# Optimization experiments

Hardware: AMD Instinct MI355X
Metric: run time of the kernel (lower is better)

Reference implementation:

```python
import jax, jax.numpy as jnp
import numpy as np

T, D, H, E = 8192, 1024, 512, 8
BLK = 32  # MXFP8 scaling block size along the contraction dim


def setup_inputs() -> dict:
    key = jax.random.key(0)
    k1, k2, k3, k4 = jax.random.split(key, 4)
    # qdata: values representable-ish in e4m3 (we use small normal floats)
    output_e4m3 = jax.random.normal(k1, (T, D), dtype=jnp.float32)
    # e8m0 scales are powers of two, one per 32-element block along dim
    output_scales_e8m0 = jnp.exp2(
        jax.random.randint(k2, (T, D // BLK), -2, 3).astype(jnp.float32)
    )
    # uniform token distribution across experts (tokens are expert-contiguous)
    num_tokens_per_expert = jnp.full((E,), T // E, dtype=jnp.int32)
    expert_padded_offsets = jnp.zeros((E,), dtype=jnp.int32)  # unused by forward body
    w13 = jax.random.normal(k3, (E, 2 * H, D), dtype=jnp.float32) * 0.02
    w2 = jax.random.normal(k4, (E, D, H), dtype=jnp.float32) * 0.02
    return {
        "output_e4m3": output_e4m3,
        "output_scales_e8m0": output_scales_e8m0,
        "num_tokens_per_expert": num_tokens_per_expert,
        "expert_padded_offsets": expert_padded_offsets,
        "w13": w13,
        "w2": w2,
    }


def reference(output_e4m3, output_scales_e8m0, num_tokens_per_expert,
              expert_padded_offsets, w13, w2):
    # Dequantize MXFP8: qdata * per-block e8m0 scale, blocks of 32 along dim.
    scales = jnp.repeat(output_scales_e8m0, BLK, axis=-1)  # [T, D]
    x = output_e4m3 * scales  # [T, D] high-precision reference activations
    # Grouped GEMM 1: tokens are expert-contiguous with uniform group sizes,
    # so the ragged grouped matmul reduces to a batched einsum per expert.
    tpe = T // E
    xg = x.reshape(E, tpe, D)                       # [E, tpe, D]
    h13 = jnp.einsum("etd,ehd->eth", xg, w13)       # [E, tpe, 2H]
    h1, h3 = h13[..., :H], h13[..., H:]
    h = jax.nn.silu(h1) * h3                        # fused SiLU-gate
    # Grouped GEMM 2
    out = jnp.einsum("eth,edh->etd", h, w2)         # [E, tpe, D]
    return out.reshape(T, D)
```

## Files before the change

### kernel.cpp

```cpp
#include <hip/hip_runtime.h>
#include <hip/hip_bf16.h>

#define T_TOK 8192
#define DDIM  1024
#define HDIM  512
#define NE    8
#define TPE   (T_TOK / NE)

typedef __attribute__((ext_vector_type(4))) float floatx4;
typedef __attribute__((ext_vector_type(8))) short bf16x8;

#define SBAR() __builtin_amdgcn_sched_barrier(0)

__device__ __forceinline__ unsigned short f2bf(float f) {
    union { float f; unsigned int u; } v;
    v.f = f;
    unsigned int u = v.u;
    unsigned int r = u + 0x7FFFu + ((u >> 16) & 1u);
    return (unsigned short)(r >> 16);
}

__device__ __forceinline__ unsigned int cvt_pk_bf16(float lo, float hi) {
    unsigned int r;
    asm("v_cvt_pk_bf16_f32 %0, %1, %2" : "=v"(r) : "v"(lo), "v"(hi));
    return r;
}

__device__ __forceinline__ void gld_lds16(const void* g, void* l) {
    __builtin_amdgcn_global_load_lds(
        (const __attribute__((address_space(1))) unsigned int*)g,
        (__attribute__((address_space(3))) unsigned int*)l, 16, 0, 0);
}

__global__ __launch_bounds__(256)
void convert_x_kernel(const float* __restrict__ X, const float* __restrict__ S,
                      unsigned short* __restrict__ Xb)
{
    const int NTX = (T_TOK * DDIM) / 4;
    const int stride = gridDim.x * blockDim.x;
    for (int i = blockIdx.x * blockDim.x + threadIdx.x; i < NTX; i += stride) {
        int row = i >> 8;
        int c4  = i & 255;
        float4 v = reinterpret_cast<const float4*>(X)[i];
        float sc = S[row * (DDIM / 32) + (c4 >> 3)];
        ushort4 b;
        b.x = f2bf(v.x * sc); b.y = f2bf(v.y * sc);
        b.z = f2bf(v.z * sc); b.w = f2bf(v.w * sc);
        reinterpret_cast<ushort4*>(Xb)[i] = b;
    }
}

__device__ __forceinline__ int xcd_swizzle_512(int raw) {
    return (raw & 7) * 64 + (raw >> 3);
}


__global__ __launch_bounds__(256, 2)
void gemm1_silu_kernel(const unsigned short* __restrict__ Xb,
                       const float* __restrict__ W13,
                       __hip_bfloat16* __restrict__ Hout)
{
    const int bid = xcd_swizzle_512(blockIdx.x);
    const int e  = bid >> 6;
    const int mt = (bid >> 3) & 7;
    const int nt = bid & 7;
    const int tok0 = e * TPE + mt * 128;
    const float* __restrict__ We = W13 + (size_t)e * (2 * HDIM) * DDIM;

    __shared__ __hip_bfloat16 sA[2][128][64];
    __shared__ __hip_bfloat16 sB[2][128][64];

    const int tid  = threadIdx.x;
    const int lane = tid & 63;
    const int wave = tid >> 6;
    const int wr = wave >> 1;
    const int wc = wave & 1;
    const int lr = lane & 15;
    const int sw0 = ((lane >> 4) ^ (lane & 7));

    floatx4 acc1[4][2] = {};
    floatx4 acc3[4][2] = {};

    const int srow0 = (tid >> 3);
    const int c8    = (tid & 7) * 8;
    const int dcol  = (tid & 7) * 8;
    const int gcol  = ((tid & 7) ^ (srow0 & 7)) * 8;
    const int swcol = gcol;

    float4 rB0[8], rB1[8];

    auto LOADB = [&](int kk, float4* rB) {
        const int k0 = kk * 64;
        #pragma unroll
        for (int j = 0; j < 4; ++j) {
            int row = srow0 + j * 32;
            int wrow = (j < 2) ? (nt * 64 + row)
                               : (HDIM + nt * 64 + (row - 64));
            const float* p = &We[(size_t)wrow * DDIM + k0 + c8];
            rB[2*j]   = *reinterpret_cast<const float4*>(p);
            rB[2*j+1] = *reinterpret_cast<const float4*>(p + 4);
        }
    };
    auto STAGEA = [&](int kk, int buf) {
        const int k0 = kk * 64;
        #pragma unroll
        for (int j = 0; j < 4; ++j) {
            int row = srow0 + j * 32;
            gld_lds16(&Xb[(size_t)(tok0 + row) * DDIM + k0 + gcol],
                      &sA[buf][row][dcol]);
        }
    };
    auto WRITEB = [&](int buf, const float4* rB) {
        #pragma unroll
        for (int j = 0; j < 4; ++j) {
            int row = srow0 + j * 32;
            uint4 w;
            w.x = cvt_pk_bf16(rB[2*j].x,   rB[2*j].y);
            w.y = cvt_pk_bf16(rB[2*j].z,   rB[2*j].w);
            w.z = cvt_pk_bf16(rB[2*j+1].x, rB[2*j+1].y);
            w.w = cvt_pk_bf16(rB[2*j+1].z, rB[2*j+1].w);
            *reinterpret_cast<uint4*>(&sB[buf][row][swcol]) = w;
        }
    };
    auto COMPUTE_KS = [&](int buf, int ks) {
        const int rc = (sw0 ^ (ks << 2)) << 3;
        bf16x8 a[4], b1[2], b3[2];
        #pragma unroll
        for (int m = 0; m < 4; ++m)
            a[m] = *reinterpret_cast<const bf16x8*>(&sA[buf][wr * 64 + m * 16 + lr][rc]);
        #pragma unroll
        for (int n = 0; n < 2; ++n) {
            b1[n] = *reinterpret_cast<const bf16x8*>(&sB[buf][wc * 32 + n * 16 + lr][rc]);
            b3[n] = *reinterpret_cast<const bf16x8*>(&sB[buf][64 + wc * 32 + n * 16 + lr][rc]);
        }
        #pragma unroll
        for (int m = 0; m < 4; ++m)
            #pragma unroll
            for (int n = 0; n < 2; ++n) {
                acc1[m][n] = __builtin_amdgcn_mfma_f32_16x16x32_bf16(a[m], b1[n], acc1[m][n], 0, 0, 0);
                acc3[m][n] = __builtin_amdgcn_mfma_f32_16x16x32_bf16(a[m], b3[n], acc3[m][n], 0, 0, 0);
            }
    };

    LOADB(0, rB0);  SBAR();
    STAGEA(0, 0);   SBAR();
    LOADB(1, rB1);  SBAR();
    asm volatile("s_waitcnt vmcnt(8)" ::: "memory");
    SBAR();
    WRITEB(0, rB0); SBAR();
    asm volatile("s_waitcnt lgkmcnt(0)" ::: "memory");
    SBAR();
    __builtin_amdgcn_s_barrier();

    for (int t = 0; t < DDIM / 64 - 2; t += 2) {
        asm volatile("s_waitcnt vmcnt(0)" ::: "memory");
        SBAR();
        WRITEB(1, rB1);     SBAR();
        STAGEA(t + 1, 1);   SBAR();
        LOADB(t + 2, rB0);  SBAR();
        COMPUTE_KS(0, 0);
        COMPUTE_KS(0, 1);
        asm volatile("s_waitcnt vmcnt(8)" ::: "memory");
        SBAR();
        __builtin_amdgcn_s_barrier();
        asm volatile("s_waitcnt vmcnt(0)" ::: "memory");
        SBAR();
        WRITEB(0, rB0);     SBAR();
        STAGEA(t + 2, 0);   SBAR();
        LOADB(t + 3, rB1);  SBAR();
        COMPUTE_KS(1, 0);
        COMPUTE_KS(1, 1);
        asm volatile("s_waitcnt vmcnt(8)" ::: "memory");
        SBAR();
        __builtin_amdgcn_s_barrier();
    }

    asm volatile("s_waitcnt vmcnt(0)" ::: "memory");
    SBAR();
    WRITEB(1, rB1);   SBAR();
    STAGEA(15, 1);    SBAR();
    COMPUTE_KS(0, 0);
    COMPUTE_KS(0, 1);
    asm volatile("s_waitcnt vmcnt(0)" ::: "memory");
    SBAR();
    __builtin_amdgcn_s_barrier();
    COMPUTE_KS(1, 0);
    COMPUTE_KS(1, 1);

    const int hcol0 = nt * 64 + wc * 32;
    #pragma unroll
    for (int m = 0; m < 4; ++m) {
        #pragma unroll
        for (int n = 0; n < 2; ++n) {
            #pragma unroll
            for (int i = 0; i < 4; ++i) {
                int row = tok0 + wr * 64 + m * 16 + (lane >> 4) * 4 + i;
                int col = hcol0 + n * 16 + (lane & 15);
                float h1 = acc1[m][n][i];
                float h3 = acc3[m][n][i];
                float sig = 1.0f / (1.0f + __expf(-h1));
                Hout[(size_t)row * HDIM + col] = __float2bfloat16(h1 * sig * h3);
            }
        }
    }
}

__global__ __launch_bounds__(256, 2)
void gemm2_kernel(const __hip_bfloat16* __restrict__ Hin,
                  const float* __restrict__ W2,
                  float* __restrict__ Out)
{
    const int bid = xcd_swizzle_512(blockIdx.x);
    const int e  = bid >> 6;
    const int nt = (bid >> 3) & 7;
    const int mt = bid & 7;
    const int tok0 = e * TPE + mt * 128;
    const float* __restrict__ We = W2 + (size_t)e * DDIM * HDIM;

    __shared__ __hip_bfloat16 sA[2][128][64];
    __shared__ __hip_bfloat16 sB[2][128][64];

    const int tid  = threadIdx.x;
    const int lane = tid & 63;
    const int wave = tid >> 6;
    const int wr = wave >> 1;
    const int wc = wave & 1;
    const int lr = lane & 15;
    const int sw0 = ((lane >> 4) ^ (lane & 7));

    floatx4 acc[4][4] = {};

    const int srow0 = (tid >> 3);
    const int c8    = (tid & 7) * 8;
    const int dcol  = (tid & 7) * 8;
    const int swcol = ((tid & 7) ^ (srow0 & 7)) * 8;

    float4 rB[8];

    auto LOADB = [&](int kk) {
        const int k0 = kk * 64;
        #pragma unroll
        for (int j = 0; j < 4; ++j) {
            int row = srow0 + j * 32;
            const float* p = &We[(size_t)(nt * 128 + row) * HDIM + k0 + c8];
            rB[2*j]   = *reinterpret_cast<const float4*>(p);
            rB[2*j+1] = *reinterpret_cast<const float4*>(p + 4);
        }
    };
    auto STAGEA = [&](int kk, int buf) {
        const int k0 = kk * 64;
        #pragma unroll
        for (int j = 0; j < 4; ++j) {
            int row = srow0 + j * 32;
            gld_lds16(&Hin[(size_t)(tok0 + row) * HDIM + k0 + swcol],
                      &sA[buf][row][dcol]);
        }
    };
    auto WRITEB = [&](int buf) {
        #pragma unroll
        for (int j = 0; j < 4; ++j) {
            int row = srow0 + j * 32;
            uint4 w;
            w.x = cvt_pk_bf16(rB[2*j].x,   rB[2*j].y);
            w.y = cvt_pk_bf16(rB[2*j].z,   rB[2*j].w);
            w.z = cvt_pk_bf16(rB[2*j+1].x, rB[2*j+1].y);
            w.w = cvt_pk_bf16(rB[2*j+1].z, rB[2*j+1].w);
            *reinterpret_cast<uint4*>(&sB[buf][row][swcol]) = w;
        }
    };
    auto COMPUTE = [&](int buf) {
        #pragma unroll
        for (int ks = 0; ks < 2; ++ks) {
            const int rc = (sw0 ^ (ks << 2)) << 3;
            bf16x8 a[4], b[4];
            #pragma unroll
            for (int m = 0; m < 4; ++m)
                a[m] = *reinterpret_cast<const bf16x8*>(&sA[buf][wr * 64 + m * 16 + lr][rc]);
            #pragma unroll
            for (int n = 0; n < 4; ++n)
                b[n] = *reinterpret_cast<const bf16x8*>(&sB[buf][wc * 64 + n * 16 + lr][rc]);
            #pragma unroll
            for (int m = 0; m < 4; ++m)
                #pragma unroll
                for (int n = 0; n < 4; ++n)
                    acc[m][n] = __builtin_amdgcn_mfma_f32_16x16x32_bf16(a[m], b[n], acc[m][n], 0, 0, 0);
        }
    };

    LOADB(0);
    __builtin_amdgcn_sched_barrier(0);
    STAGEA(0, 0);
    __builtin_amdgcn_sched_barrier(0);
    for (int kk = 0; kk < HDIM / 64 - 1; ++kk) {
        const int buf = kk & 1;
        asm volatile("s_waitcnt vmcnt(4)" ::: "memory");
        __builtin_amdgcn_sched_barrier(0);
        WRITEB(buf);
        __builtin_amdgcn_sched_barrier(0);
        LOADB(kk + 1);
        __builtin_amdgcn_sched_barrier(0);
        STAGEA(kk + 1, buf ^ 1);
        __builtin_amdgcn_sched_barrier(0);
        asm volatile("s_waitcnt vmcnt(12) lgkmcnt(0)" ::: "memory");
        __builtin_amdgcn_sched_barrier(0);
        __builtin_amdgcn_s_barrier();
        COMPUTE(buf);
        __builtin_amdgcn_s_barrier();
    }
    asm volatile("s_waitcnt vmcnt(4)" ::: "memory");
    __builtin_amdgcn_sched_barrier(0);
    WRITEB(1);
    asm volatile("s_waitcnt vmcnt(0) lgkmcnt(0)" ::: "memory");
    __builtin_amdgcn_sched_barrier(0);
    __builtin_amdgcn_s_barrier();
    COMPUTE(1);

    const int dcol0 = nt * 128 + wc * 64;
    #pragma unroll
    for (int m = 0; m < 4; ++m) {
        #pragma unroll
        for (int n = 0; n < 4; ++n) {
            #pragma unroll
            for (int i = 0; i < 4; ++i) {
                int row = tok0 + wr * 64 + m * 16 + (lane >> 4) * 4 + i;
                int col = dcol0 + n * 16 + (lane & 15);
                Out[(size_t)row * DDIM + col] = acc[m][n][i];
            }
        }
    }
}

extern "C" void kernel_launch(void* const* d_in, const int* in_sizes, int n_in,
                              void* d_out, int out_size, void* d_ws, size_t ws_size,
                              hipStream_t stream) {
    const float* X   = (const float*)d_in[0];
    const float* S   = (const float*)d_in[1];
    const float* W13 = (const float*)d_in[4];
    const float* W2  = (const float*)d_in[5];
    float* Out = (float*)d_out;

    __hip_bfloat16* Hb = (__hip_bfloat16*)d_ws;
    unsigned short* Xb = (unsigned short*)d_out;

    convert_x_kernel<<<2048, 256, 0, stream>>>(X, S, Xb);
    gemm1_silu_kernel<<<NE * 8 * 8, 256, 0, stream>>>(Xb, W13, Hb);
    gemm2_kernel<<<NE * 8 * 8, 256, 0, stream>>>(Hb, W2, Out);
}
```

Baseline: 55.84 us.

## Deepen software pipeline: move B register-to-LDS writes after compute in both GEMMs

In the first GEMM, the conversion and LDS write of prefetched B tiles moves from before the MFMA block to after it. Each wait only drains the loads it needs (vmcnt 12/8) instead of fully draining. The second GEMM is rewritten to the same double-register-buffered two-stage scheme, prefetching B two tiles ahead and removing one barrier per iteration. The aim is to hide global load latency behind MFMA work, at the cost of more registers for the second B buffer and more delicate wait counts.

```diff
diff --git a/kernel.cpp b/kernel.cpp
--- a/kernel.cpp
+++ b/kernel.cpp
@@ -145,43 +145,43 @@
     LOADB(0, rB0);  SBAR();
     STAGEA(0, 0);   SBAR();
     LOADB(1, rB1);  SBAR();
-    asm volatile("s_waitcnt vmcnt(8)" ::: "memory");
+    asm volatile("s_waitcnt vmcnt(12)" ::: "memory");
     SBAR();
     WRITEB(0, rB0); SBAR();
-    asm volatile("s_waitcnt lgkmcnt(0)" ::: "memory");
+    asm volatile("s_waitcnt vmcnt(8) lgkmcnt(0)" ::: "memory");
     SBAR();
     __builtin_amdgcn_s_barrier();
 
     for (int t = 0; t < DDIM / 64 - 2; t += 2) {
-        asm volatile("s_waitcnt vmcnt(0)" ::: "memory");
-        SBAR();
-        WRITEB(1, rB1);     SBAR();
         STAGEA(t + 1, 1);   SBAR();
         LOADB(t + 2, rB0);  SBAR();
         COMPUTE_KS(0, 0);
         COMPUTE_KS(0, 1);
-        asm volatile("s_waitcnt vmcnt(8)" ::: "memory");
+        asm volatile("s_waitcnt vmcnt(12)" ::: "memory");
+        SBAR();
+        WRITEB(1, rB1);     SBAR();
+        asm volatile("s_waitcnt vmcnt(8) lgkmcnt(0)" ::: "memory");
         SBAR();
         __builtin_amdgcn_s_barrier();
-        asm volatile("s_waitcnt vmcnt(0)" ::: "memory");
-        SBAR();
-        WRITEB(0, rB0);     SBAR();
         STAGEA(t + 2, 0);   SBAR();
         LOADB(t + 3, rB1);  SBAR();
         COMPUTE_KS(1, 0);
         COMPUTE_KS(1, 1);
-        asm volatile("s_waitcnt vmcnt(8)" ::: "memory");
+        asm volatile("s_waitcnt vmcnt(12)" ::: "memory");
+        SBAR();
+        WRITEB(0, rB0);     SBAR();
+        asm volatile("s_waitcnt vmcnt(8) lgkmcnt(0)" ::: "memory");
         SBAR();
         __builtin_amdgcn_s_barrier();
     }
 
-    asm volatile("s_waitcnt vmcnt(0)" ::: "memory");
-    SBAR();
-    WRITEB(1, rB1);   SBAR();
     STAGEA(15, 1);    SBAR();
     COMPUTE_KS(0, 0);
     COMPUTE_KS(0, 1);
-    asm volatile("s_waitcnt vmcnt(0)" ::: "memory");
+    asm volatile("s_waitcnt vmcnt(4)" ::: "memory");
+    SBAR();
+    WRITEB(1, rB1);   SBAR();
+    asm volatile("s_waitcnt vmcnt(0) lgkmcnt(0)" ::: "memory");
     SBAR();
     __builtin_amdgcn_s_barrier();
     COMPUTE_KS(1, 0);
@@ -235,9 +235,9 @@
     const int dcol  = (tid & 7) * 8;
     const int swcol = ((tid & 7) ^ (srow0 & 7)) * 8;
 
-    float4 rB[8];
-
-    auto LOADB = [&](int kk) {
+    float4 rB0[8], rB1[8];
+
+    auto LOADB = [&](int kk, float4* rB) {
         const int k0 = kk * 64;
         #pragma unroll
         for (int j = 0; j < 4; ++j) {
@@ -256,7 +256,7 @@
                       &sA[buf][row][dcol]);
         }
     };
-    auto WRITEB = [&](int buf) {
+    auto WRITEB = [&](int buf, const float4* rB) {
         #pragma unroll
         for (int j = 0; j < 4; ++j) {
             int row = srow0 + j * 32;
@@ -287,31 +287,44 @@
         }
     };
 
-    LOADB(0);
-    __builtin_amdgcn_sched_barrier(0);
-    STAGEA(0, 0);
-    __builtin_amdgcn_sched_barrier(0);
-    for (int kk = 0; kk < HDIM / 64 - 1; ++kk) {
-        const int buf = kk & 1;
-        asm volatile("s_waitcnt vmcnt(4)" ::: "memory");
-        __builtin_amdgcn_sched_barrier(0);
-        WRITEB(buf);
-        __builtin_amdgcn_sched_barrier(0);
-        LOADB(kk + 1);
-        __builtin_amdgcn_sched_barrier(0);
-        STAGEA(kk + 1, buf ^ 1);
-        __builtin_amdgcn_sched_barrier(0);
-        asm volatile("s_waitcnt vmcnt(12) lgkmcnt(0)" ::: "memory");
-        __builtin_amdgcn_sched_barrier(0);
+    LOADB(0, rB0);  SBAR();
+    STAGEA(0, 0);   SBAR();
+    LOADB(1, rB1);  SBAR();
+    asm volatile("s_waitcnt vmcnt(12)" ::: "memory");
+    SBAR();
+    WRITEB(0, rB0); SBAR();
+    asm volatile("s_waitcnt vmcnt(8) lgkmcnt(0)" ::: "memory");
+    SBAR();
+    __builtin_amdgcn_s_barrier();
+
+    for (int t = 0; t < HDIM / 64 - 2; t += 2) {
+        STAGEA(t + 1, 1);   SBAR();
+        LOADB(t + 2, rB0);  SBAR();
+        COMPUTE(0);
+        asm volatile("s_waitcnt vmcnt(12)" ::: "memory");
+        SBAR();
+        WRITEB(1, rB1);     SBAR();
+        asm volatile("s_waitcnt vmcnt(8) lgkmcnt(0)" ::: "memory");
+        SBAR();
         __builtin_amdgcn_s_barrier();
-        COMPUTE(buf);
+        STAGEA(t + 2, 0);   SBAR();
+        LOADB(t + 3, rB1);  SBAR();
+        COMPUTE(1);
+        asm volatile("s_waitcnt vmcnt(12)" ::: "memory");
+        SBAR();
+        WRITEB(0, rB0);     SBAR();
+        asm volatile("s_waitcnt vmcnt(8) lgkmcnt(0)" ::: "memory");
+        SBAR();
         __builtin_amdgcn_s_barrier();
     }
+
+    STAGEA(7, 1);   SBAR();
+    COMPUTE(0);
     asm volatile("s_waitcnt vmcnt(4)" ::: "memory");
-    __builtin_amdgcn_sched_barrier(0);
-    WRITEB(1);
+    SBAR();
+    WRITEB(1, rB1); SBAR();
     asm volatile("s_waitcnt vmcnt(0) lgkmcnt(0)" ::: "memory");
-    __builtin_amdgcn_sched_barrier(0);
+    SBAR();
     __builtin_amdgcn_s_barrier();
     COMPUTE(1);
 
```

New measurement: 55.91 us. About the same (+0.1%).
